# Kernel optimization log

Hardware: AMD Instinct MI355X
Metric: run time of the kernel (lower is better)

Reference implementation:

```python
import jax, jax.numpy as jnp
import numpy as np

HIDDEN = 512
ATT_DIM = 128
LN_EPS = 1e-3  # keras LayerNormalization default epsilon


def setup_inputs() -> dict:
    key = jax.random.key(0)
    k1, k2, k3, k4 = jax.random.split(key, 4)
    hidden_states = jax.random.normal(k1, (64, 2048, HIDDEN), dtype=jnp.float32)
    # Glorot-uniform style init for the dense weights
    def glorot(k, shape):
        lim = np.sqrt(6.0 / (shape[0] + shape[1]))
        return jax.random.uniform(k, shape, jnp.float32, -lim, lim)
    W_a = glorot(k2, (HIDDEN, ATT_DIM))
    U_a = glorot(k3, (HIDDEN, ATT_DIM))
    v_a = glorot(k4, (ATT_DIM, 1))
    ln_gamma = jnp.ones((HIDDEN,), jnp.float32)
    ln_beta = jnp.zeros((HIDDEN,), jnp.float32)
    return {"hidden_states": hidden_states, "W_a": W_a, "U_a": U_a,
            "v_a": v_a, "ln_gamma": ln_gamma, "ln_beta": ln_beta}


def reference(hidden_states, W_a, U_a, v_a, ln_gamma, ln_beta):
    # hidden_states: (B, L, H)
    h_att = jnp.einsum('blh,ha->bla', hidden_states, W_a)        # (B, L, A)
    context = jnp.mean(hidden_states, axis=1, keepdims=True)     # (B, 1, H)
    u_att = jnp.einsum('blh,ha->bla', context, U_a)              # (B, 1, A) broadcasts
    combined = jnp.tanh(h_att + u_att)                           # (B, L, A)
    scores = jnp.einsum('bla,ao->bl', combined, v_a)             # (B, L)
    attn = jax.nn.softmax(scores, axis=-1)                       # (B, L)
    attended = jnp.einsum('blh,bl->bh', hidden_states, attn)     # (B, H)
    # LayerNormalization over last axis
    mu = jnp.mean(attended, axis=-1, keepdims=True)
    var = jnp.var(attended, axis=-1, keepdims=True)
    normed = (attended - mu) * jax.lax.rsqrt(var + LN_EPS)
    out = normed * ln_gamma + ln_beta
    return out, attn
```

## Files before the change

kernel.cpp:

```cpp
#include <hip/hip_runtime.h>
#include <hip/hip_bf16.h>

#define HIDDEN 512
#define ATT    128
#define NB     64
#define SL     2048
#define LN_EPS 1e-3f

typedef __attribute__((ext_vector_type(8))) short short8;
typedef __attribute__((ext_vector_type(4))) short short4v;
typedef __attribute__((ext_vector_type(4))) float f32x4;

__device__ __forceinline__ short f2bf(float f) {
    union { float f; unsigned u; } v; v.f = f;
    unsigned r = v.u + 0x7fffu + ((v.u >> 16) & 1u);
    return (short)(r >> 16);
}
__device__ __forceinline__ float bf2f(short b) {
    union { unsigned u; float f; } v;
    v.u = ((unsigned)(unsigned short)b) << 16; return v.f;
}
__device__ __forceinline__ float tanh_fast(float x) {
    float cx = fminf(fmaxf(x, -15.f), 15.f);
    float e = __expf(2.f * cx);
    return (e - 1.f) * __builtin_amdgcn_rcpf(e + 1.f);
}

__global__ void p0_wt(const float* __restrict__ W, short* __restrict__ Wt) {
    int idx = blockIdx.x * 256 + threadIdx.x;
    int a = idx >> 9, h = idx & 511;
    Wt[idx] = f2bf(W[h * ATT + a]);
}

__launch_bounds__(256)
__global__ void p1_gemm_ctx(const float* __restrict__ hidden, const short* __restrict__ Wt,
                            short* __restrict__ h_att, float* __restrict__ ctx_part) {
    __shared__ float ctx_s[HIDDEN];
    __shared__ short out_s[128 * 136];

    int t = threadIdx.x;
    int row0 = blockIdx.x * 128;
    int wave = t >> 6, lane = t & 63, quad = lane >> 4, cb = lane & 15;

    ctx_s[t] = 0.f; ctx_s[t + 256] = 0.f;
    __syncthreads();

    f32x4 acc[2][8];
    #pragma unroll
    for (int mt = 0; mt < 2; ++mt)
        #pragma unroll
        for (int nt = 0; nt < 8; ++nt)
            acc[mt][nt] = (f32x4){0.f, 0.f, 0.f, 0.f};

    const float* aptr0 = hidden + (size_t)(row0 + wave * 32 + cb) * HIDDEN;
    const float* aptr1 = aptr0 + (size_t)16 * HIDDEN;
    const short* bptr  = Wt + (size_t)cb * HIDDEN;

    for (int k0 = 0; k0 < HIDDEN; k0 += 32) {
        int ka = k0 + quad * 8;
        const float4 a0lo = *(const float4*)(aptr0 + ka);
        const float4 a0hi = *(const float4*)(aptr0 + ka + 4);
        const float4 a1lo = *(const float4*)(aptr1 + ka);
        const float4 a1hi = *(const float4*)(aptr1 + ka + 4);

        short8 b8[8];
        #pragma unroll
        for (int nt = 0; nt < 8; ++nt)
            b8[nt] = *(const short8*)(bptr + nt * 16 * HIDDEN + ka);

        float s[8] = { a0lo.x + a1lo.x, a0lo.y + a1lo.y, a0lo.z + a1lo.z, a0lo.w + a1lo.w,
                       a0hi.x + a1hi.x, a0hi.y + a1hi.y, a0hi.z + a1hi.z, a0hi.w + a1hi.w };
        #pragma unroll
        for (int j = 0; j < 8; ++j) {
            s[j] += __shfl_xor(s[j], 1);
            s[j] += __shfl_xor(s[j], 2);
            s[j] += __shfl_xor(s[j], 4);
            s[j] += __shfl_xor(s[j], 8);
        }
        if (cb == 0) {
            #pragma unroll
            for (int j = 0; j < 8; ++j) atomicAdd(&ctx_s[ka + j], s[j]);
        }

        short8 a0 = { f2bf(a0lo.x), f2bf(a0lo.y), f2bf(a0lo.z), f2bf(a0lo.w),
                      f2bf(a0hi.x), f2bf(a0hi.y), f2bf(a0hi.z), f2bf(a0hi.w) };
        short8 a1 = { f2bf(a1lo.x), f2bf(a1lo.y), f2bf(a1lo.z), f2bf(a1lo.w),
                      f2bf(a1hi.x), f2bf(a1hi.y), f2bf(a1hi.z), f2bf(a1hi.w) };

        #pragma unroll
        for (int nt = 0; nt < 8; ++nt) {
            acc[0][nt] = __builtin_amdgcn_mfma_f32_16x16x32_bf16(a0, b8[nt], acc[0][nt], 0, 0, 0);
            acc[1][nt] = __builtin_amdgcn_mfma_f32_16x16x32_bf16(a1, b8[nt], acc[1][nt], 0, 0, 0);
        }
    }
    __syncthreads();
    ctx_part[(size_t)blockIdx.x * HIDDEN + t]       = ctx_s[t];
    ctx_part[(size_t)blockIdx.x * HIDDEN + 256 + t] = ctx_s[t + 256];

    #pragma unroll
    for (int mt = 0; mt < 2; ++mt)
        #pragma unroll
        for (int nt = 0; nt < 8; ++nt)
            #pragma unroll
            for (int j = 0; j < 4; ++j)
                out_s[(wave * 32 + mt * 16 + quad * 4 + j) * 136 + nt * 16 + cb] = f2bf(acc[mt][nt][j]);
    __syncthreads();
    {
        int row = t >> 1, seg = t & 1;
        const short* srcp = out_s + row * 136 + seg * 64;
        short8* dstp = (short8*)(h_att + ((size_t)(row0 + row)) * ATT + seg * 64);
        #pragma unroll
        for (int i = 0; i < 8; ++i) dstp[i] = *(const short8*)(srcp + i * 8);
    }
}

__launch_bounds__(256)
__global__ void p2_uatt(const float* __restrict__ ctx_part, const float* __restrict__ U,
                        float* __restrict__ uatt) {
    int b = blockIdx.x, t = threadIdx.x;
    __shared__ float cs[HIDDEN];
    float s0 = 0.f, s1 = 0.f;
    #pragma unroll
    for (int c = 0; c < 16; ++c) {
        size_t base = (size_t)(b * 16 + c) * HIDDEN;
        s0 += ctx_part[base + t];
        s1 += ctx_part[base + 256 + t];
    }
    cs[t] = s0; cs[t + 256] = s1;
    __syncthreads();
    if (t < ATT) {
        float d = 0.f;
        #pragma unroll 8
        for (int h = 0; h < HIDDEN; ++h) d += cs[h] * U[h * ATT + t];
        uatt[b * ATT + t] = d * (1.f / SL);
    }
}

__launch_bounds__(256)
__global__ void p3_scores(const short* __restrict__ h_att, const float* __restrict__ v_a,
                          const float* __restrict__ uatt, float* __restrict__ scores) {
    int t = threadIdx.x, bx = blockIdx.x;
    int row0 = bx * 64, b = bx >> 5;
    __shared__ float v_s[ATT], u_s[ATT];
    if (t < ATT) { v_s[t] = v_a[t]; u_s[t] = uatt[b * ATT + t]; }
    __syncthreads();
    int lr = t >> 2, seg = t & 3;
    const short8* p = (const short8*)(h_att + ((size_t)(row0 + lr)) * ATT + seg * 32);
    float s = 0.f;
    #pragma unroll
    for (int q = 0; q < 4; ++q) {
        short8 h8 = p[q];
        #pragma unroll
        for (int i = 0; i < 8; ++i) {
            int a = seg * 32 + q * 8 + i;
            s += v_s[a] * tanh_fast(bf2f(h8[i]) + u_s[a]);
        }
    }
    s += __shfl_xor(s, 1);
    s += __shfl_xor(s, 2);
    if (seg == 0) scores[row0 + lr] = s;
}

__launch_bounds__(256)
__global__ void p4_softmax(float* __restrict__ attn) {
    int b = blockIdx.x, t = threadIdx.x;
    float* p = attn + b * SL;
    __shared__ float red[256];
    float v[8];
    float m = -1e30f;
    #pragma unroll
    for (int i = 0; i < 8; ++i) { v[i] = p[t + i * 256]; m = fmaxf(m, v[i]); }
    red[t] = m; __syncthreads();
    for (int s = 128; s > 0; s >>= 1) { if (t < s) red[t] = fmaxf(red[t], red[t + s]); __syncthreads(); }
    m = red[0]; __syncthreads();
    float sum = 0.f;
    #pragma unroll
    for (int i = 0; i < 8; ++i) { v[i] = __expf(v[i] - m); sum += v[i]; }
    red[t] = sum; __syncthreads();
    for (int s = 128; s > 0; s >>= 1) { if (t < s) red[t] += red[t + s]; __syncthreads(); }
    float inv = 1.f / red[0];
    #pragma unroll
    for (int i = 0; i < 8; ++i) p[t + i * 256] = v[i] * inv;
}

__launch_bounds__(256)
__global__ void p5_attended(const float* __restrict__ hidden, const float* __restrict__ attn,
                            float* __restrict__ att_part) {
    int b = blockIdx.y, c = blockIdx.x, t = threadIdx.x;
    __shared__ float w_s[128];
    __shared__ float4 red_s[128];
    if (t < 128) w_s[t] = attn[b * SL + c * 128 + t];
    __syncthreads();
    int cg = t & 127, half = t >> 7;
    const float* hp = hidden + ((size_t)b * SL + c * 128 + half * 64) * HIDDEN + cg * 4;
    float4 a = {0.f, 0.f, 0.f, 0.f};
    #pragma unroll 4
    for (int l = 0; l < 64; ++l) {
        float w = w_s[half * 64 + l];
        const float4 g = *(const float4*)(hp + (size_t)l * HIDDEN);
        a.x += w * g.x; a.y += w * g.y; a.z += w * g.z; a.w += w * g.w;
    }
    if (half) red_s[cg] = a;
    __syncthreads();
    if (!half) {
        float4 r = red_s[cg];
        a.x += r.x; a.y += r.y; a.z += r.z; a.w += r.w;
        *(float4*)(att_part + ((size_t)(c * NB + b)) * HIDDEN + cg * 4) = a;
    }
}

__launch_bounds__(256)
__global__ void p6_ln(const float* __restrict__ att_part, const float* __restrict__ gamma,
                      const float* __restrict__ beta, float* __restrict__ out) {
    int b = blockIdx.x, t = threadIdx.x;
    float x0 = 0.f, x1 = 0.f;
    #pragma unroll
    for (int c = 0; c < 16; ++c) {
        size_t base = (size_t)(c * NB + b) * HIDDEN;
        x0 += att_part[base + t];
        x1 += att_part[base + t + 256];
    }
    __shared__ float rs[256], rq[256];
    rs[t] = x0 + x1; rq[t] = x0 * x0 + x1 * x1;
    __syncthreads();
    for (int s = 128; s > 0; s >>= 1) {
        if (t < s) { rs[t] += rs[t + s]; rq[t] += rq[t + s]; }
        __syncthreads();
    }
    float mean = rs[0] * (1.f / HIDDEN);
    float var = rq[0] * (1.f / HIDDEN) - mean * mean;
    float r = rsqrtf(var + LN_EPS);
    out[b * HIDDEN + t]       = (x0 - mean) * r * gamma[t] + beta[t];
    out[b * HIDDEN + t + 256] = (x1 - mean) * r * gamma[t + 256] + beta[t + 256];
}

extern "C" void kernel_launch(void* const* d_in, const int* in_sizes, int n_in,
                              void* d_out, int out_size, void* d_ws, size_t ws_size,
                              hipStream_t stream) {
    const float* hidden = (const float*)d_in[0];
    const float* W      = (const float*)d_in[1];
    const float* U      = (const float*)d_in[2];
    const float* v_a    = (const float*)d_in[3];
    const float* gamma  = (const float*)d_in[4];
    const float* beta   = (const float*)d_in[5];

    float* out  = (float*)d_out;
    float* attn = out + NB * HIDDEN;

    short* h_att    = (short*)d_ws;
    float* ctx_part = (float*)((char*)d_ws + (size_t)NB * SL * ATT * 2);
    float* att_part = ctx_part + (size_t)1024 * HIDDEN;
    float* uatt     = att_part + (size_t)16 * NB * HIDDEN;
    short* Wt       = (short*)(uatt + NB * ATT);

    p0_wt<<<256, 256, 0, stream>>>(W, Wt);
    p1_gemm_ctx<<<(NB * SL) / 128, 256, 0, stream>>>(hidden, Wt, h_att, ctx_part);
    p2_uatt<<<NB, 256, 0, stream>>>(ctx_part, U, uatt);
    p3_scores<<<(NB * SL) / 64, 256, 0, stream>>>(h_att, v_a, uatt, attn);
    p4_softmax<<<NB, 256, 0, stream>>>(attn);
    p5_attended<<<dim3(16, NB), 256, 0, stream>>>(hidden, attn, att_part);
    p6_ln<<<NB, 256, 0, stream>>>(att_part, gamma, beta, out);
}
```

Baseline: 495.9 us.

## Store GEMM output in MFMA fragment layout and drop LDS staging

The GEMM kernel now writes its bf16 h_att tile straight from the MFMA accumulator layout to global memory in a fragment-native order. This removes the shared-memory transpose and the extra barriers. The score kernel is rewritten to read that same fragment layout and reduce with shuffles. Per-wave context partial sums are written directly instead of going through LDS atomics, so the uatt kernel now sums 64 partials per batch and splits the U dot product across all 256 threads. The GEMM also uses packed bf16 conversion, unroll 2 and an occupancy hint, at the cost of a larger context-partial workspace.

```diff
diff --git a/kernel.cpp b/kernel.cpp
--- a/kernel.cpp
+++ b/kernel.cpp
@@ -8,7 +8,6 @@
 #define LN_EPS 1e-3f
 
 typedef __attribute__((ext_vector_type(8))) short short8;
-typedef __attribute__((ext_vector_type(4))) short short4v;
 typedef __attribute__((ext_vector_type(4))) float f32x4;
 
 __device__ __forceinline__ short f2bf(float f) {
@@ -16,9 +15,16 @@
     unsigned r = v.u + 0x7fffu + ((v.u >> 16) & 1u);
     return (short)(r >> 16);
 }
-__device__ __forceinline__ float bf2f(short b) {
-    union { unsigned u; float f; } v;
-    v.u = ((unsigned)(unsigned short)b) << 16; return v.f;
+__device__ __forceinline__ unsigned pack2bf(float lo, float hi) {
+    union { __hip_bfloat162 h; unsigned u; } v;
+    v.h = __float22bfloat162_rn(make_float2(lo, hi));
+    return v.u;
+}
+__device__ __forceinline__ float bflo(unsigned u) {
+    union { unsigned x; float f; } v; v.x = u << 16; return v.f;
+}
+__device__ __forceinline__ float bfhi(unsigned u) {
+    union { unsigned x; float f; } v; v.x = u & 0xffff0000u; return v.f;
 }
 __device__ __forceinline__ float tanh_fast(float x) {
     float cx = fminf(fmaxf(x, -15.f), 15.f);
@@ -32,18 +38,12 @@
     Wt[idx] = f2bf(W[h * ATT + a]);
 }
 
-__launch_bounds__(256)
+__launch_bounds__(256, 3)
 __global__ void p1_gemm_ctx(const float* __restrict__ hidden, const short* __restrict__ Wt,
                             short* __restrict__ h_att, float* __restrict__ ctx_part) {
-    __shared__ float ctx_s[HIDDEN];
-    __shared__ short out_s[128 * 136];
-
     int t = threadIdx.x;
+    int wave = t >> 6, lane = t & 63, quad = lane >> 4, cb = lane & 15;
     int row0 = blockIdx.x * 128;
-    int wave = t >> 6, lane = t & 63, quad = lane >> 4, cb = lane & 15;
-
-    ctx_s[t] = 0.f; ctx_s[t + 256] = 0.f;
-    __syncthreads();
 
     f32x4 acc[2][8];
     #pragma unroll
@@ -52,21 +52,22 @@
         for (int nt = 0; nt < 8; ++nt)
             acc[mt][nt] = (f32x4){0.f, 0.f, 0.f, 0.f};
 
-    const float* aptr0 = hidden + (size_t)(row0 + wave * 32 + cb) * HIDDEN;
+    const float* aptr0 = hidden + (size_t)(row0 + wave * 32 + cb) * HIDDEN + quad * 8;
     const float* aptr1 = aptr0 + (size_t)16 * HIDDEN;
-    const short* bptr  = Wt + (size_t)cb * HIDDEN;
-
+    const short* bptr  = Wt + (size_t)cb * HIDDEN + quad * 8;
+    float* cptr = ctx_part + (size_t)(blockIdx.x * 4 + wave) * HIDDEN + quad * 8;
+
+    #pragma unroll 2
     for (int k0 = 0; k0 < HIDDEN; k0 += 32) {
-        int ka = k0 + quad * 8;
-        const float4 a0lo = *(const float4*)(aptr0 + ka);
-        const float4 a0hi = *(const float4*)(aptr0 + ka + 4);
-        const float4 a1lo = *(const float4*)(aptr1 + ka);
-        const float4 a1hi = *(const float4*)(aptr1 + ka + 4);
+        const float4 a0lo = *(const float4*)(aptr0 + k0);
+        const float4 a0hi = *(const float4*)(aptr0 + k0 + 4);
+        const float4 a1lo = *(const float4*)(aptr1 + k0);
+        const float4 a1hi = *(const float4*)(aptr1 + k0 + 4);
 
         short8 b8[8];
         #pragma unroll
         for (int nt = 0; nt < 8; ++nt)
-            b8[nt] = *(const short8*)(bptr + nt * 16 * HIDDEN + ka);
+            b8[nt] = *(const short8*)(bptr + nt * 16 * HIDDEN + k0);
 
         float s[8] = { a0lo.x + a1lo.x, a0lo.y + a1lo.y, a0lo.z + a1lo.z, a0lo.w + a1lo.w,
                        a0hi.x + a1hi.x, a0hi.y + a1hi.y, a0hi.z + a1hi.z, a0hi.w + a1hi.w };
@@ -79,39 +80,33 @@
         }
         if (cb == 0) {
             #pragma unroll
-            for (int j = 0; j < 8; ++j) atomicAdd(&ctx_s[ka + j], s[j]);
-        }
-
-        short8 a0 = { f2bf(a0lo.x), f2bf(a0lo.y), f2bf(a0lo.z), f2bf(a0lo.w),
-                      f2bf(a0hi.x), f2bf(a0hi.y), f2bf(a0hi.z), f2bf(a0hi.w) };
-        short8 a1 = { f2bf(a1lo.x), f2bf(a1lo.y), f2bf(a1lo.z), f2bf(a1lo.w),
-                      f2bf(a1hi.x), f2bf(a1hi.y), f2bf(a1hi.z), f2bf(a1hi.w) };
+            for (int j = 0; j < 8; ++j) cptr[k0 + j] = s[j];
+        }
+
+        union { short8 s8; unsigned u[4]; } a0p, a1p;
+        a0p.u[0] = pack2bf(a0lo.x, a0lo.y); a0p.u[1] = pack2bf(a0lo.z, a0lo.w);
+        a0p.u[2] = pack2bf(a0hi.x, a0hi.y); a0p.u[3] = pack2bf(a0hi.z, a0hi.w);
+        a1p.u[0] = pack2bf(a1lo.x, a1lo.y); a1p.u[1] = pack2bf(a1lo.z, a1lo.w);
+        a1p.u[2] = pack2bf(a1hi.x, a1hi.y); a1p.u[3] = pack2bf(a1hi.z, a1hi.w);
 
         #pragma unroll
         for (int nt = 0; nt < 8; ++nt) {
-            acc[0][nt] = __builtin_amdgcn_mfma_f32_16x16x32_bf16(a0, b8[nt], acc[0][nt], 0, 0, 0);
-            acc[1][nt] = __builtin_amdgcn_mfma_f32_16x16x32_bf16(a1, b8[nt], acc[1][nt], 0, 0, 0);
-        }
-    }
-    __syncthreads();
-    ctx_part[(size_t)blockIdx.x * HIDDEN + t]       = ctx_s[t];
-    ctx_part[(size_t)blockIdx.x * HIDDEN + 256 + t] = ctx_s[t + 256];
-
+            acc[0][nt] = __builtin_amdgcn_mfma_f32_16x16x32_bf16(a0p.s8, b8[nt], acc[0][nt], 0, 0, 0);
+            acc[1][nt] = __builtin_amdgcn_mfma_f32_16x16x32_bf16(a1p.s8, b8[nt], acc[1][nt], 0, 0, 0);
+        }
+    }
+
+    uint2* hp = (uint2*)h_att;
+    size_t base = (((size_t)blockIdx.x * 4 + wave) * 2) * 8 * 64 + lane;
     #pragma unroll
     for (int mt = 0; mt < 2; ++mt)
         #pragma unroll
-        for (int nt = 0; nt < 8; ++nt)
-            #pragma unroll
-            for (int j = 0; j < 4; ++j)
-                out_s[(wave * 32 + mt * 16 + quad * 4 + j) * 136 + nt * 16 + cb] = f2bf(acc[mt][nt][j]);
-    __syncthreads();
-    {
-        int row = t >> 1, seg = t & 1;
-        const short* srcp = out_s + row * 136 + seg * 64;
-        short8* dstp = (short8*)(h_att + ((size_t)(row0 + row)) * ATT + seg * 64);
-        #pragma unroll
-        for (int i = 0; i < 8; ++i) dstp[i] = *(const short8*)(srcp + i * 8);
-    }
+        for (int nt = 0; nt < 8; ++nt) {
+            uint2 p;
+            p.x = pack2bf(acc[mt][nt][0], acc[mt][nt][1]);
+            p.y = pack2bf(acc[mt][nt][2], acc[mt][nt][3]);
+            hp[base + ((size_t)mt * 8 + nt) * 64] = p;
+        }
 }
 
 __launch_bounds__(256)
@@ -119,46 +114,69 @@
                         float* __restrict__ uatt) {
     int b = blockIdx.x, t = threadIdx.x;
     __shared__ float cs[HIDDEN];
+    __shared__ float ds[256];
     float s0 = 0.f, s1 = 0.f;
-    #pragma unroll
-    for (int c = 0; c < 16; ++c) {
-        size_t base = (size_t)(b * 16 + c) * HIDDEN;
-        s0 += ctx_part[base + t];
-        s1 += ctx_part[base + 256 + t];
+    #pragma unroll 4
+    for (int c = 0; c < 64; ++c) {
+        const float* base = ctx_part + (size_t)(b * 64 + c) * HIDDEN;
+        s0 += base[t];
+        s1 += base[t + 256];
     }
     cs[t] = s0; cs[t + 256] = s1;
     __syncthreads();
-    if (t < ATT) {
-        float d = 0.f;
-        #pragma unroll 8
-        for (int h = 0; h < HIDDEN; ++h) d += cs[h] * U[h * ATT + t];
-        uatt[b * ATT + t] = d * (1.f / SL);
-    }
+    int a = t & 127, h0 = (t >> 7) * 256;
+    float d = 0.f;
+    #pragma unroll 8
+    for (int h = 0; h < 256; ++h) d += cs[h0 + h] * U[(size_t)(h0 + h) * ATT + a];
+    ds[t] = d;
+    __syncthreads();
+    if (t < 128) uatt[b * ATT + t] = (ds[t] + ds[t + 128]) * (1.f / SL);
 }
 
 __launch_bounds__(256)
 __global__ void p3_scores(const short* __restrict__ h_att, const float* __restrict__ v_a,
                           const float* __restrict__ uatt, float* __restrict__ scores) {
     int t = threadIdx.x, bx = blockIdx.x;
-    int row0 = bx * 64, b = bx >> 5;
-    __shared__ float v_s[ATT], u_s[ATT];
-    if (t < ATT) { v_s[t] = v_a[t]; u_s[t] = uatt[b * ATT + t]; }
-    __syncthreads();
-    int lr = t >> 2, seg = t & 3;
-    const short8* p = (const short8*)(h_att + ((size_t)(row0 + lr)) * ATT + seg * 32);
-    float s = 0.f;
-    #pragma unroll
-    for (int q = 0; q < 4; ++q) {
-        short8 h8 = p[q];
-        #pragma unroll
-        for (int i = 0; i < 8; ++i) {
-            int a = seg * 32 + q * 8 + i;
-            s += v_s[a] * tanh_fast(bf2f(h8[i]) + u_s[a]);
-        }
-    }
-    s += __shfl_xor(s, 1);
-    s += __shfl_xor(s, 2);
-    if (seg == 0) scores[row0 + lr] = s;
+    int wave = t >> 6, lane = t & 63, quad = lane >> 4, cb = lane & 15;
+    int b = bx >> 4;
+    int row0 = bx * 128;
+
+    float uv[8], vv[8];
+    #pragma unroll
+    for (int nt = 0; nt < 8; ++nt) {
+        uv[nt] = uatt[b * ATT + nt * 16 + cb];
+        vv[nt] = v_a[nt * 16 + cb];
+    }
+
+    const uint2* hp = (const uint2*)h_att;
+    size_t base = (((size_t)bx * 4 + wave) * 2) * 8 * 64 + lane;
+
+    #pragma unroll
+    for (int mt = 0; mt < 2; ++mt) {
+        uint2 f[8];
+        #pragma unroll
+        for (int nt = 0; nt < 8; ++nt) f[nt] = hp[base + ((size_t)mt * 8 + nt) * 64];
+        float r[4] = {0.f, 0.f, 0.f, 0.f};
+        #pragma unroll
+        for (int nt = 0; nt < 8; ++nt) {
+            r[0] += vv[nt] * tanh_fast(bflo(f[nt].x) + uv[nt]);
+            r[1] += vv[nt] * tanh_fast(bfhi(f[nt].x) + uv[nt]);
+            r[2] += vv[nt] * tanh_fast(bflo(f[nt].y) + uv[nt]);
+            r[3] += vv[nt] * tanh_fast(bfhi(f[nt].y) + uv[nt]);
+        }
+        #pragma unroll
+        for (int j = 0; j < 4; ++j) {
+            r[j] += __shfl_xor(r[j], 1);
+            r[j] += __shfl_xor(r[j], 2);
+            r[j] += __shfl_xor(r[j], 4);
+            r[j] += __shfl_xor(r[j], 8);
+        }
+        if (cb == 0) {
+            #pragma unroll
+            for (int j = 0; j < 4; ++j)
+                scores[row0 + wave * 32 + mt * 16 + quad * 4 + j] = r[j];
+        }
+    }
 }
 
 __launch_bounds__(256)
@@ -249,14 +267,14 @@
 
     short* h_att    = (short*)d_ws;
     float* ctx_part = (float*)((char*)d_ws + (size_t)NB * SL * ATT * 2);
-    float* att_part = ctx_part + (size_t)1024 * HIDDEN;
+    float* att_part = ctx_part + (size_t)4096 * HIDDEN;
     float* uatt     = att_part + (size_t)16 * NB * HIDDEN;
     short* Wt       = (short*)(uatt + NB * ATT);
 
     p0_wt<<<256, 256, 0, stream>>>(W, Wt);
     p1_gemm_ctx<<<(NB * SL) / 128, 256, 0, stream>>>(hidden, Wt, h_att, ctx_part);
     p2_uatt<<<NB, 256, 0, stream>>>(ctx_part, U, uatt);
-    p3_scores<<<(NB * SL) / 64, 256, 0, stream>>>(h_att, v_a, uatt, attn);
+    p3_scores<<<(NB * SL) / 128, 256, 0, stream>>>(h_att, v_a, uatt, attn);
     p4_softmax<<<NB, 256, 0, stream>>>(attn);
     p5_attended<<<dim3(16, NB), 256, 0, stream>>>(hidden, attn, att_part);
     p6_ln<<<NB, 256, 0, stream>>>(att_part, gamma, beta, out);
```

Measured after the change: 504.1 us. Within noise of the previous version (+1.7%).
